# Optimization experiments

Hardware: AMD Instinct MI355X
Metric: run time of the kernel (lower is better)

Reference implementation:

```python
import jax, jax.numpy as jnp
import numpy as np

H = 256          # hidden_dim
B = 64           # molecules
M = 64           # atoms per molecule (equal-size molecules)
N = B * M        # total nodes
NE = 119         # element classes
NB = 5           # bond classes
EPS = 1e-5
OFF_I, OFF_J = np.where(~np.eye(M, dtype=bool))  # static off-diagonal pair order (i-major, j!=i)


def _gelu(x):
    return jax.nn.gelu(x, approximate=False)


def _ln(x, g, b):
    mu = jnp.mean(x, axis=-1, keepdims=True)
    var = jnp.mean((x - mu) ** 2, axis=-1, keepdims=True)
    return (x - mu) * jax.lax.rsqrt(var + EPS) * g + b


def _mlp(x, W1, b1, g, bn, W2, b2, W3, b3):
    x = _gelu(x @ W1 + b1)
    x = _ln(x, g, bn)
    x = _gelu(x @ W2 + b2)
    return x @ W3 + b3


def setup_inputs():
    key = jax.random.key(0)
    ks = jax.random.split(key, 16)
    s = 0.02
    def lin(k, fi, fo):
        return jax.random.normal(k, (fi, fo), jnp.float32) * s
    inp = {}
    inp["h"] = jax.random.normal(ks[0], (N, H), jnp.float32)
    inp["pos"] = jax.random.normal(ks[1], (N, 3), jnp.float32) * 3.0
    inp["edge_index"] = jax.random.randint(ks[2], (2, N * 8), 0, N)
    inp["batch"] = jnp.repeat(jnp.arange(B), M)
    # atom_predictor params
    inp["aW1"] = lin(ks[3], H, H); inp["ab1"] = jnp.zeros((H,))
    inp["ag"] = jnp.ones((H,)); inp["abn"] = jnp.zeros((H,))
    inp["aW2"] = lin(ks[4], H, H // 2); inp["ab2"] = jnp.zeros((H // 2,))
    inp["aW3"] = lin(ks[5], H // 2, NE); inp["ab3"] = jnp.zeros((NE,))
    # valency_predictor params
    inp["vW1"] = lin(ks[6], H + NE, H); inp["vb1"] = jnp.zeros((H,))
    inp["vg"] = jnp.ones((H,)); inp["vbn"] = jnp.zeros((H,))
    inp["vW2"] = lin(ks[7], H, H // 2); inp["vb2"] = jnp.zeros((H // 2,))
    inp["vW3"] = lin(ks[8], H // 2, 1); inp["vb3"] = jnp.zeros((1,))
    # bond_predictor params
    inp["bW1"] = lin(ks[9], 2 * H + 4, H); inp["bb1"] = jnp.zeros((H,))
    inp["bg"] = jnp.ones((H,)); inp["bbn"] = jnp.zeros((H,))
    inp["bW2"] = lin(ks[10], H, H // 2); inp["bb2"] = jnp.zeros((H // 2,))
    inp["bW3"] = lin(ks[11], H // 2, NB); inp["bb3"] = jnp.zeros((NB,))
    # chemical constant buffers (stand-ins for RDKit tables)
    mv = np.ones(NE, np.float32) * 4.0
    mv[[1, 9, 17, 35, 53]] = 1.0; mv[8] = 2.0; mv[7] = 3.0; mv[16] = 6.0; mv[15] = 5.0
    inp["max_valences"] = jnp.asarray(mv)
    cr = np.ones(NE, np.float32) * 1.5
    cr[1] = 0.31; cr[6] = 0.76; cr[7] = 0.71; cr[8] = 0.66; cr[9] = 0.57; cr[16] = 1.05
    inp["covalent_radii"] = jnp.asarray(cr)
    return inp


def _forward(h, pos, aW1, ab1, ag, abn, aW2, ab2, aW3, ab3,
             vW1, vb1, vg, vbn, vW2, vb2, vW3, vb3,
             bW1, bb1, bg, bbn, bW2, bb2, bW3, bb3,
             max_valences, covalent_radii):
    atom_logits = _mlp(h, aW1, ab1, ag, abn, aW2, ab2, aW3, ab3)        # [N,119]
    atom_probs = jax.nn.softmax(atom_logits, axis=-1)
    val = _mlp(jnp.concatenate([h, atom_probs], -1), vW1, vb1, vg, vbn, vW2, vb2, vW3, vb3)
    val = jax.nn.softplus(val)                                          # [N,1]
    pred = jnp.clip(jnp.argmax(atom_probs, -1), 0, 118)
    max_allowed = max_valences[pred]                                    # [N]
    # torch.min([N], [N,1]) broadcasts to [N,N] in the original -- reproduced faithfully
    valency_constrained = jnp.minimum(val[:, 0], max_allowed[:, None])  # [N,N]
    # vectorized pairwise bond prediction per molecule (equal-size molecules)
    hB = h.reshape(B, M, H)
    pB = pos.reshape(B, M, 3)
    probsB = atom_probs.reshape(B, M, NE)
    dist = jnp.linalg.norm(pB[:, :, None, :] - pB[:, None, :, :], axis=-1)  # [B,M,M]
    radii = covalent_radii[jnp.minimum(jnp.argmax(probsB, -1), 118)]        # [B,M]
    expected = radii[:, :, None] + radii[:, None, :]                        # [B,M,M]
    close = (dist < 3.0).astype(h.dtype)
    feats = jnp.concatenate([
        jnp.broadcast_to(hB[:, :, None, :], (B, M, M, H)),
        jnp.broadcast_to(hB[:, None, :, :], (B, M, M, H)),
        dist[..., None], expected[..., None],
        (dist / expected)[..., None], close[..., None],
    ], axis=-1)                                                             # [B,M,M,2H+4]
    logits = _mlp(feats, bW1, bb1, bg, bbn, bW2, bb2, bW3, bb3)             # [B,M,M,5]
    probs5 = jax.nn.softmax(logits, axis=-1)
    e0 = jnp.zeros((NB,), h.dtype).at[0].set(1.0)
    diag = jnp.eye(M, dtype=bool)[None, :, :, None]
    adjacency = jnp.where(diag, e0, probs5)                                 # [B,M,M,5]
    bond_logits = logits[:, OFF_I, OFF_J, :].reshape(B * M * (M - 1), NB)   # skip i==j, i-major order
    return (atom_logits, bond_logits, valency_constrained, adjacency)


def reference(h, pos, edge_index, batch, aW1, ab1, ag, abn, aW2, ab2, aW3, ab3,
              vW1, vb1, vg, vbn, vW2, vb2, vW3, vb3,
              bW1, bb1, bg, bbn, bW2, bb2, bW3, bb3, max_valences, covalent_radii):
    # edge_index is unused by the original forward; batch is implicit in the [B,M] layout
    return _forward(h, pos, aW1, ab1, ag, abn, aW2, ab2, aW3, ab3,
                    vW1, vb1, vg, vbn, vW2, vb2, vW3, vb3,
                    bW1, bb1, bg, bbn, bW2, bb2, bW3, bb3,
                    max_valences, covalent_radii)
```

## Files before the change

### kernel.cpp

```cpp
#include <hip/hip_runtime.h>
#include <math.h>

#define NN   4096
#define HH   256
#define NEC  119
#define NBC  5

#define OFF_ATOM   0
#define OFF_BOND   487424
#define OFF_VALM   (487424+1290240)
#define OFF_ADJ    (1777664+16777216)

typedef short  bf16x8 __attribute__((ext_vector_type(8)));
typedef float  f32x4  __attribute__((ext_vector_type(4)));

__device__ __forceinline__ float gelu_f(float x) {
    float z = fabsf(x) * 0.70710678118654752f;
    float t = __builtin_amdgcn_rcpf(fmaf(0.3275911f, z, 1.0f));
    float p = t * fmaf(t, fmaf(t, fmaf(t, fmaf(t, 1.061405429f, -1.453152027f),
                                       1.421413741f), -0.284496736f), 0.254829592f);
    float er = fmaf(-p, __expf(-z * z), 1.0f);
    float s = copysignf(er, x);
    return 0.5f * x * (1.f + s);
}
__device__ __forceinline__ unsigned short f2bf(float x) {
    unsigned int u = __float_as_uint(x);
    unsigned int r = (u + 0x7fffu + ((u >> 16) & 1u)) >> 16;
    return (unsigned short)r;
}

__global__ __launch_bounds__(256) void k_prep(
    const float* __restrict__ bW1, const float* __restrict__ bW2,
    const float* __restrict__ bW3, const float* __restrict__ vW1,
    const float* __restrict__ vW2,
    const float* __restrict__ bg, const float* __restrict__ bbn,
    const float* __restrict__ bb2,
    short* __restrict__ PQf, short* __restrict__ V1f, short* __restrict__ V2vf,
    short* __restrict__ W2f, short* __restrict__ W3f,
    float* __restrict__ uu, float* __restrict__ vvb)
{
    const int t = threadIdx.x;
    if (blockIdx.x == 1160) {
        if (t < 128) {
            float ua = 0.f, va = 0.f;
            for (int c = 0; c < 256; ++c) {
                float w = bW2[c * 128 + t];
                ua = fmaf(bg[c],  w, ua);
                va = fmaf(bbn[c], w, va);
            }
            uu[t]  = ua;
            vvb[t] = va + bb2[t];
        }
        return;
    }
    const int id = blockIdx.x * 256 + t;
    if (id < 131072) {
        const int e = id & 7, l = (id >> 3) & 63;
        const int rem = id >> 9, ks = rem & 7, ct = rem >> 3;
        const int k = ks * 32 + (l >> 4) * 8 + e;
        const int col = ct * 16 + (l & 15);
        float v = (col < 256) ? bW1[k * 256 + col] : bW1[(256 + k) * 256 + (col - 256)];
        PQf[id] = (short)f2bf(v);
    } else if (id < 229376) {
        const int id2 = id - 131072;
        const int e = id2 & 7, l = (id2 >> 3) & 63;
        const int rem = id2 >> 9, ks = rem % 12, ct = rem / 12;
        const int kk = ks * 32 + (l >> 4) * 8 + e;
        const int col = ct * 16 + (l & 15);
        V1f[id2] = (kk < 375) ? (short)f2bf(vW1[kk * 256 + col]) : (short)0;
    } else if (id < 262144) {
        const int id3 = id - 229376;
        const int e = id3 & 7, l = (id3 >> 3) & 63;
        const int rem = id3 >> 9, ks = rem & 7, ct = rem >> 3;
        const int k = ks * 32 + (l >> 4) * 8 + e;
        const int col = ct * 16 + (l & 15);
        V2vf[id3] = (short)f2bf(vW2[k * 128 + col]);
    } else if (id < 294912) {
        const int id4 = id - 262144;
        const int e = id4 & 7, l = (id4 >> 3) & 63;
        const int ks = (id4 >> 9) & 7, ct = (id4 >> 12) & 7;
        const int k = ks * 32 + (l >> 4) * 8 + e;
        const int col = ct * 16 + (l & 15);
        W2f[id4] = (short)f2bf(bW2[k * 128 + col]);
    } else if (id < 296960) {
        const int id5 = id - 294912;
        const int e = id5 & 7, l = (id5 >> 3) & 63, ks = id5 >> 9;
        const int k = ks * 32 + (l >> 4) * 8 + e;
        const int col = l & 15;
        W3f[id5] = (col < NBC) ? (short)f2bf(bW3[k * NBC + col]) : (short)0;
    }
}

__global__ __launch_bounds__(256, 3) void k_front(
    const float* __restrict__ h,
    const float* __restrict__ aW1, const float* __restrict__ ab1,
    const float* __restrict__ ag,  const float* __restrict__ abn,
    const float* __restrict__ aW2, const float* __restrict__ ab2,
    const float* __restrict__ aW3, const float* __restrict__ ab3,
    const float* __restrict__ maxv, const float* __restrict__ covr,
    const float* __restrict__ vb1, const float* __restrict__ vg,
    const float* __restrict__ vbn, const float* __restrict__ vb2,
    const float* __restrict__ vW3, const float* __restrict__ vb3,
    const float* __restrict__ bb1,
    const short* __restrict__ PQf, const short* __restrict__ V1f,
    const short* __restrict__ V2vf,
    float* __restrict__ logits_out,
    float* __restrict__ ma, float* __restrict__ rad, float* __restrict__ val,
    float* __restrict__ P, float* __restrict__ Q)
{
    __shared__ __align__(16) char smem[44864];
    float (*hs)[256]   = (float(*)[256])(smem);
    unsigned short* hb = (unsigned short*)(smem + 8192);
    float (*z1)[256]   = (float(*)[256])(smem + 20480);
    float (*z2)[128]   = (float(*)[128])(smem + 28672);
    float (*llog)[120] = (float(*)[120])(smem + 32768);
    unsigned short* zb = (unsigned short*)(smem + 36608);
    float (*redbuf)[2] = (float(*)[2])(smem + 44800);

    const int t  = threadIdx.x;
    const int wv = t >> 6, ln = t & 63;
    const int lr = ln & 15, kg = ln >> 4;

    if (blockIdx.x >= 512) {
        unsigned short* hbq = (unsigned short*)smem;
        const int gb  = blockIdx.x - 512;
        const int rt  = gb & 63, ct4 = gb >> 6;
        const int n0  = rt * 64, c0 = ct4 * 64;

        for (int i = 0; i < 16; ++i) {
            const int idx4 = t + 256 * i;
            const int r = idx4 >> 6, k4 = (idx4 & 63) * 4;
            float4 hv = *(const float4*)(h + (size_t)(n0 + r) * 256 + k4);
            ushort4 u;
            u.x = f2bf(hv.x); u.y = f2bf(hv.y); u.z = f2bf(hv.z); u.w = f2bf(hv.w);
            const int off = r * 512 + ((((k4 >> 3) ^ (r & 7))) << 4) + ((k4 & 7) << 1);
            *(ushort4*)((char*)hbq + off) = u;
        }
        __syncthreads();

        const int wr0 = wv * 16;
        f32x4 acc[4];
        #pragma unroll
        for (int ctl = 0; ctl < 4; ++ctl) acc[ctl] = (f32x4){0.f, 0.f, 0.f, 0.f};
        #pragma unroll
        for (int ks = 0; ks < 8; ++ks) {
            const int row = wr0 + lr;
            const int chunk = ks * 4 + kg;
            const int aoff = row * 512 + ((chunk ^ (row & 7)) << 4);
            bf16x8 afr = *(const bf16x8*)((char*)hbq + aoff);
            #pragma unroll
            for (int ctl = 0; ctl < 4; ++ctl) {
                const int ct_pq = ct4 * 4 + ctl;
                bf16x8 bfr = *(const bf16x8*)(PQf + (((size_t)(ct_pq * 8 + ks)) * 64 + ln) * 8);
                acc[ctl] = __builtin_amdgcn_mfma_f32_16x16x32_bf16(afr, bfr, acc[ctl], 0, 0, 0);
            }
        }
        #pragma unroll
        for (int ctl = 0; ctl < 4; ++ctl) {
            const int colg = c0 + ctl * 16 + lr;
            const float bias = (colg < 256) ? bb1[colg] : 0.f;
            #pragma unroll
            for (int r = 0; r < 4; ++r) {
                const int n = n0 + wr0 + kg * 4 + r;
                float v = acc[ctl][r] + bias;
                if (colg < 256) P[(size_t)n * 256 + colg] = v;
                else            Q[(size_t)n * 256 + (colg - 256)] = v;
            }
        }
        return;
    }

    const int n0 = blockIdx.x * 8;

    #pragma unroll
    for (int i = 0; i < 3; ++i)
        *(int4*)((char*)hb + (t + 256 * i) * 16) = (int4){0, 0, 0, 0};
    *(int4*)((char*)zb + 4096 + t * 16) = (int4){0, 0, 0, 0};
    for (int i = 0; i < 2; ++i) {
        const int idx4 = t + 256 * i;
        const int r = idx4 >> 6, k4 = (idx4 & 63) * 4;
        float4 hv = *(const float4*)(h + (size_t)(n0 + r) * 256 + k4);
        *(float4*)&hs[r][k4] = hv;
        ushort4 u;
        u.x = f2bf(hv.x); u.y = f2bf(hv.y); u.z = f2bf(hv.z); u.w = f2bf(hv.w);
        const int off = r * 768 + ((((k4 >> 3) ^ (r & 7))) << 4) + ((k4 & 7) << 1);
        *(ushort4*)((char*)hb + off) = u;
    }
    __syncthreads();

    {
        const int c = t;
        float b1 = ab1[c];
        float acc[8];
        #pragma unroll
        for (int r = 0; r < 8; ++r) acc[r] = b1;
        for (int k4 = 0; k4 < 64; ++k4) {
            const int k = k4 * 4;
            float w0 = aW1[(k + 0) * 256 + c];
            float w1 = aW1[(k + 1) * 256 + c];
            float w2 = aW1[(k + 2) * 256 + c];
            float w3 = aW1[(k + 3) * 256 + c];
            #pragma unroll
            for (int r = 0; r < 8; ++r) {
                float4 hv = *(const float4*)&hs[r][k];
                acc[r] = fmaf(hv.x, w0, acc[r]);
                acc[r] = fmaf(hv.y, w1, acc[r]);
                acc[r] = fmaf(hv.z, w2, acc[r]);
                acc[r] = fmaf(hv.w, w3, acc[r]);
            }
        }
        #pragma unroll
        for (int r = 0; r < 8; ++r) z1[r][c] = gelu_f(acc[r]);
    }
    __syncthreads();

    for (int rr = 0; rr < 2; ++rr) {
        const int r = wv * 2 + rr;
        float s = 0.f, s2 = 0.f;
        #pragma unroll
        for (int q = 0; q < 4; ++q) {
            float v = z1[r][ln + q * 64];
            s += v; s2 = fmaf(v, v, s2);
        }
        #pragma unroll
        for (int m = 32; m >= 1; m >>= 1) {
            s  += __shfl_xor(s,  m, 64);
            s2 += __shfl_xor(s2, m, 64);
        }
        if (ln == 0) {
            float mu  = s * (1.f / 256.f);
            float var = s2 * (1.f / 256.f) - mu * mu;
            redbuf[r][0] = mu;
            redbuf[r][1] = rsqrtf(var + 1e-5f);
        }
    }
    __syncthreads();
    {
        const int c = t;
        float g = ag[c], b = abn[c];
        #pragma unroll
        for (int r = 0; r < 8; ++r)
            z1[r][c] = (z1[r][c] - redbuf[r][0]) * redbuf[r][1] * g + b;
    }
    __syncthreads();

    {
        const int c2 = t & 127, kh = t >> 7;
        float acc2[8];
        #pragma unroll
        for (int r = 0; r < 8; ++r) acc2[r] = 0.f;
        const int kb = kh * 128;
        for (int k4 = 0; k4 < 32; ++k4) {
            const int k = kb + k4 * 4;
            float w0 = aW2[(k + 0) * 128 + c2];
            float w1 = aW2[(k + 1) * 128 + c2];
            float w2 = aW2[(k + 2) * 128 + c2];
            float w3 = aW2[(k + 3) * 128 + c2];
            #pragma unroll
            for (int r = 0; r < 8; ++r) {
                float4 zv = *(const float4*)&z1[r][k];
                acc2[r] = fmaf(zv.x, w0, acc2[r]);
                acc2[r] = fmaf(zv.y, w1, acc2[r]);
                acc2[r] = fmaf(zv.z, w2, acc2[r]);
                acc2[r] = fmaf(zv.w, w3, acc2[r]);
            }
        }
        if (kh == 1) {
            #pragma unroll
            for (int r = 0; r < 8; ++r) z2[r][c2] = acc2[r];
        }
        __syncthreads();
        if (kh == 0) {
            float b2 = ab2[c2];
            #pragma unroll
            for (int r = 0; r < 8; ++r)
                z2[r][c2] = gelu_f(acc2[r] + z2[r][c2] + b2);
        }
    }
    __syncthreads();

    if (t < NEC) {
        const int c = t;
        float b3 = ab3[c];
        float acc3[8];
        #pragma unroll
        for (int r = 0; r < 8; ++r) acc3[r] = b3;
        for (int k4 = 0; k4 < 32; ++k4) {
            const int k = k4 * 4;
            float w0 = aW3[(k + 0) * NEC + c];
            float w1 = aW3[(k + 1) * NEC + c];
            float w2 = aW3[(k + 2) * NEC + c];
            float w3 = aW3[(k + 3) * NEC + c];
            #pragma unroll
            for (int r = 0; r < 8; ++r) {
                float4 zv = *(const float4*)&z2[r][k];
                acc3[r] = fmaf(zv.x, w0, acc3[r]);
                acc3[r] = fmaf(zv.y, w1, acc3[r]);
                acc3[r] = fmaf(zv.z, w2, acc3[r]);
                acc3[r] = fmaf(zv.w, w3, acc3[r]);
            }
        }
        #pragma unroll
        for (int r = 0; r < 8; ++r) {
            llog[r][c] = acc3[r];
            logits_out[(size_t)(n0 + r) * NEC + c] = acc3[r];
        }
    }
    __syncthreads();

    for (int rr = 0; rr < 2; ++rr) {
        const int r = wv * 2 + rr;
        float v1 = llog[r][ln];
        float v2 = (ln + 64 < NEC) ? llog[r][ln + 64] : -1e30f;
        float mx; int mi;
        if (v2 > v1) { mx = v2; mi = ln + 64; } else { mx = v1; mi = ln; }
        #pragma unroll
        for (int m = 32; m >= 1; m >>= 1) {
            float ov = __shfl_xor(mx, m, 64);
            int   oi = __shfl_xor(mi, m, 64);
            if (ov > mx || (ov == mx && oi < mi)) { mx = ov; mi = oi; }
        }
        float e1 = __expf(v1 - mx);
        float e2 = (ln + 64 < NEC) ? __expf(v2 - mx) : 0.f;
        float s = e1 + e2;
        #pragma unroll
        for (int m = 32; m >= 1; m >>= 1) s += __shfl_xor(s, m, 64);
        float inv = __builtin_amdgcn_rcpf(s);
        {
            const int cf = 256 + ln;
            const int off = r * 768 + ((((cf >> 3) ^ (r & 7))) << 4) + ((cf & 7) << 1);
            *(unsigned short*)((char*)hb + off) = f2bf(e1 * inv);
        }
        if (ln + 64 < NEC) {
            const int cf = 256 + ln + 64;
            const int off = r * 768 + ((((cf >> 3) ^ (r & 7))) << 4) + ((cf & 7) << 1);
            *(unsigned short*)((char*)hb + off) = f2bf(e2 * inv);
        }
        if (ln == 0) {
            ma[n0 + r]  = maxv[mi];
            rad[n0 + r] = covr[mi];
        }
    }
    __syncthreads();

    {
        f32x4 acc[4];
        #pragma unroll
        for (int ctl = 0; ctl < 4; ++ctl) acc[ctl] = (f32x4){0.f, 0.f, 0.f, 0.f};
        #pragma unroll
        for (int ks = 0; ks < 12; ++ks) {
            const int row = lr;
            const int chunk = ks * 4 + kg;
            const int aoff = row * 768 + ((chunk ^ (row & 7)) << 4);
            bf16x8 afr = *(const bf16x8*)((char*)hb + aoff);
            #pragma unroll
            for (int ctl = 0; ctl < 4; ++ctl) {
                const int ctg = wv * 4 + ctl;
                bf16x8 bfr = *(const bf16x8*)(V1f + (((size_t)(ctg * 12 + ks)) * 64 + ln) * 8);
                acc[ctl] = __builtin_amdgcn_mfma_f32_16x16x32_bf16(afr, bfr, acc[ctl], 0, 0, 0);
            }
        }
        if (kg < 2) {
            #pragma unroll
            for (int ctl = 0; ctl < 4; ++ctl) {
                const int col = (wv * 4 + ctl) * 16 + lr;
                const float b1 = vb1[col];
                #pragma unroll
                for (int r = 0; r < 4; ++r)
                    z1[kg * 4 + r][col] = gelu_f(acc[ctl][r] + b1);
            }
        }
    }
    __syncthreads();

    for (int rr = 0; rr < 2; ++rr) {
        const int r = wv * 2 + rr;
        float s = 0.f, s2 = 0.f;
        #pragma unroll
        for (int q = 0; q < 4; ++q) {
            float v = z1[r][ln + q * 64];
            s += v; s2 = fmaf(v, v, s2);
        }
        #pragma unroll
        for (int m = 32; m >= 1; m >>= 1) {
            s  += __shfl_xor(s,  m, 64);
            s2 += __shfl_xor(s2, m, 64);
        }
        if (ln == 0) {
            float mu  = s * (1.f / 256.f);
            float var = s2 * (1.f / 256.f) - mu * mu;
            redbuf[r][0] = mu;
            redbuf[r][1] = rsqrtf(var + 1e-5f);
        }
    }
    __syncthreads();
    {
        const int c = t;
        float g = vg[c], b = vbn[c];
        #pragma unroll
        for (int r = 0; r < 8; ++r) {
            float v = (z1[r][c] - redbuf[r][0]) * redbuf[r][1] * g + b;
            const int off = r * 512 + ((((c >> 3) ^ (r & 7))) << 4) + ((c & 7) << 1);
            *(unsigned short*)((char*)zb + off) = f2bf(v);
        }
    }
    __syncthreads();

    {
        f32x4 acc2[2];
        #pragma unroll
        for (int c2 = 0; c2 < 2; ++c2) acc2[c2] = (f32x4){0.f, 0.f, 0.f, 0.f};
        #pragma unroll
        for (int ks = 0; ks < 8; ++ks) {
            const int row = lr;
            const int chunk = ks * 4 + kg;
            const int aoff = row * 512 + ((chunk ^ (row & 7)) << 4);
            bf16x8 afr = *(const bf16x8*)((char*)zb + aoff);
            #pragma unroll
            for (int c2 = 0; c2 < 2; ++c2) {
                const int ctg = wv * 2 + c2;
                bf16x8 bfr = *(const bf16x8*)(V2vf + (((size_t)(ctg * 8 + ks)) * 64 + ln) * 8);
                acc2[c2] = __builtin_amdgcn_mfma_f32_16x16x32_bf16(afr, bfr, acc2[c2], 0, 0, 0);
            }
        }
        if (kg < 2) {
            #pragma unroll
            for (int c2 = 0; c2 < 2; ++c2) {
                const int col = (wv * 2 + c2) * 16 + lr;
                const float b2 = vb2[col];
                #pragma unroll
                for (int r = 0; r < 4; ++r)
                    z2[kg * 4 + r][col] = gelu_f(acc2[c2][r] + b2);
            }
        }
    }
    __syncthreads();

    for (int rr = 0; rr < 2; ++rr) {
        const int r = wv * 2 + rr;
        float p = fmaf(z2[r][ln], vW3[ln], z2[r][ln + 64] * vW3[ln + 64]);
        #pragma unroll
        for (int m = 32; m >= 1; m >>= 1) p += __shfl_xor(p, m, 64);
        if (ln == 0) {
            float x = p + vb3[0];
            val[n0 + r] = (x > 15.f) ? x : log1pf(expf(x));
        }
    }
}

__global__ __launch_bounds__(256, 4) void k_back(
    const float* __restrict__ pos, const float* __restrict__ rad,
    const float* __restrict__ P, const float* __restrict__ Q,
    const float* __restrict__ bW1, const float* __restrict__ bg,
    const short* __restrict__ W2f, const short* __restrict__ W3f,
    const float* __restrict__ bb3,
    const float* __restrict__ uu, const float* __restrict__ vvb,
    const float* __restrict__ val, const float* __restrict__ ma,
    float* __restrict__ bond_logits, float* __restrict__ adjacency,
    float* __restrict__ valmat)
{
    __shared__ float posr[64][4];
    __shared__ float Pis[256];
    __shared__ float wst0[256], wst1[256], wst2[256], wst3[256];
    __shared__ float gams[256];
    __shared__ float us_[128], vbs[128];
    __shared__ unsigned short Ys[64 * 128];
    __shared__ float Ls[64][5];

    const int t  = threadIdx.x;

    if (blockIdx.x >= 4096) {
        const int i0 = (blockIdx.x - 4096) * 8;
        const float4* v4 = (const float4*)val;
        for (int rr = 0; rr < 8; ++rr) {
            const int i = i0 + rr;
            const float mi = ma[i];
            float4* o4 = (float4*)(valmat + (size_t)i * 4096);
            for (int j = t; j < 1024; j += 256) {
                float4 v = v4[j];
                float4 r;
                r.x = fminf(v.x, mi); r.y = fminf(v.y, mi);
                r.z = fminf(v.z, mi); r.w = fminf(v.w, mi);
                o4[j] = r;
            }
        }
        return;
    }

    const int bi = blockIdx.x;
    const int b  = bi >> 6, i = bi & 63;
    const int wv = t >> 6, ln = t & 63;
    const int lr = ln & 15, kg = ln >> 4;
    const int node0 = b * 64;
    const int j = wv * 16 + lr;

    if (t < 64) {
        int n = node0 + t;
        posr[t][0] = pos[n * 3 + 0];
        posr[t][1] = pos[n * 3 + 1];
        posr[t][2] = pos[n * 3 + 2];
        posr[t][3] = rad[n];
    }
    Pis[t]  = P[(size_t)(node0 + i) * 256 + t];
    wst0[t] = bW1[(size_t)512 * 256 + t];
    wst1[t] = bW1[(size_t)513 * 256 + t];
    wst2[t] = bW1[(size_t)514 * 256 + t];
    wst3[t] = bW1[(size_t)515 * 256 + t];
    gams[t] = bg[t];
    if (t < 128) { us_[t] = uu[t]; vbs[t] = vvb[t]; }
    __syncthreads();

    float dx = posr[i][0] - posr[j][0];
    float dy = posr[i][1] - posr[j][1];
    float dz = posr[i][2] - posr[j][2];
    float dist  = sqrtf(fmaf(dx, dx, fmaf(dy, dy, dz * dz)));
    float expd  = posr[i][3] + posr[j][3];
    float ratio = dist * __builtin_amdgcn_rcpf(expd);
    float close = (dist < 3.f) ? 1.f : 0.f;

    float s = 0.f, s2 = 0.f;
    bf16x8 afr[8];
    const float* Qrow = Q + (size_t)(node0 + j) * 256;
    #pragma unroll
    for (int ks = 0; ks < 8; ++ks) {
        const int base = ks * 32 + kg * 8;
        float4 Pa  = *(const float4*)&Pis[base],  Pb  = *(const float4*)&Pis[base + 4];
        float4 Qa  = *(const float4*)(Qrow + base), Qb = *(const float4*)(Qrow + base + 4);
        float4 w0a = *(const float4*)&wst0[base], w0b = *(const float4*)&wst0[base + 4];
        float4 w1a = *(const float4*)&wst1[base], w1b = *(const float4*)&wst1[base + 4];
        float4 w2a = *(const float4*)&wst2[base], w2b = *(const float4*)&wst2[base + 4];
        float4 w3a = *(const float4*)&wst3[base], w3b = *(const float4*)&wst3[base + 4];
        float4 ga  = *(const float4*)&gams[base], gb  = *(const float4*)&gams[base + 4];
        float g, xg;
        #define LANECH(P_, Q_, W0_, W1_, W2_, W3_, G_, EI) \
            g = P_ + Q_; g = fmaf(W0_, dist, g); g = fmaf(W1_, expd, g); \
            g = fmaf(W2_, ratio, g); g = fmaf(W3_, close, g); g = gelu_f(g); \
            s += g; s2 = fmaf(g, g, s2); xg = g * G_; afr[ks][EI] = (short)f2bf(xg);
        LANECH(Pa.x, Qa.x, w0a.x, w1a.x, w2a.x, w3a.x, ga.x, 0)
        LANECH(Pa.y, Qa.y, w0a.y, w1a.y, w2a.y, w3a.y, ga.y, 1)
        LANECH(Pa.z, Qa.z, w0a.z, w1a.z, w2a.z, w3a.z, ga.z, 2)
        LANECH(Pa.w, Qa.w, w0a.w, w1a.w, w2a.w, w3a.w, ga.w, 3)
        LANECH(Pb.x, Qb.x, w0b.x, w1b.x, w2b.x, w3b.x, gb.x, 4)
        LANECH(Pb.y, Qb.y, w0b.y, w1b.y, w2b.y, w3b.y, gb.y, 5)
        LANECH(Pb.z, Qb.z, w0b.z, w1b.z, w2b.z, w3b.z, gb.z, 6)
        LANECH(Pb.w, Qb.w, w0b.w, w1b.w, w2b.w, w3b.w, gb.w, 7)
        #undef LANECH
    }
    s  += __shfl_xor(s,  16, 64);  s  += __shfl_xor(s,  32, 64);
    s2 += __shfl_xor(s2, 16, 64);  s2 += __shfl_xor(s2, 32, 64);
    const float mu   = s * (1.f / 256.f);
    const float rstd = rsqrtf(s2 * (1.f / 256.f) - mu * mu + 1e-5f);

    f32x4 acc[8];
    #pragma unroll
    for (int ct = 0; ct < 8; ++ct) acc[ct] = (f32x4){0.f, 0.f, 0.f, 0.f};
    #pragma unroll
    for (int ks = 0; ks < 8; ++ks) {
        #pragma unroll
        for (int ct = 0; ct < 8; ++ct) {
            bf16x8 bfr = *(const bf16x8*)(W2f + (((size_t)(ct * 8 + ks)) * 64 + ln) * 8);
            acc[ct] = __builtin_amdgcn_mfma_f32_16x16x32_bf16(afr[ks], bfr, acc[ct], 0, 0, 0);
        }
    }

    float rst[4], rm[4];
    #pragma unroll
    for (int r = 0; r < 4; ++r) {
        float sr = __shfl(rstd, kg * 4 + r, 64);
        float mr = __shfl(mu,   kg * 4 + r, 64);
        rst[r] = sr; rm[r] = sr * mr;
    }
    #pragma unroll
    for (int ct = 0; ct < 8; ++ct) {
        const int col = ct * 16 + lr;
        const float ucv = us_[col], vcv = vbs[col];
        #pragma unroll
        for (int r = 0; r < 4; ++r) {
            float y = fmaf(rst[r], acc[ct][r], fmaf(-rm[r], ucv, vcv));
            y = gelu_f(y);
            const int row = wv * 16 + kg * 4 + r;
            const int chunk = col >> 3;
            const int off = row * 256 + ((chunk ^ (row & 7)) << 4) + ((col & 7) << 1);
            *(unsigned short*)((char*)Ys + off) = f2bf(y);
        }
    }

    {
        f32x4 acc3 = (f32x4){0.f, 0.f, 0.f, 0.f};
        #pragma unroll
        for (int ks = 0; ks < 4; ++ks) {
            bf16x8 bfr = *(const bf16x8*)(W3f + ((size_t)(ks * 64 + ln)) * 8);
            const int row   = wv * 16 + lr;
            const int chunk = ks * 4 + kg;
            const int off   = row * 256 + ((chunk ^ (row & 7)) << 4);
            bf16x8 afr2 = *(const bf16x8*)((char*)Ys + off);
            acc3 = __builtin_amdgcn_mfma_f32_16x16x32_bf16(afr2, bfr, acc3, 0, 0, 0);
        }
        if (lr < NBC) {
            #pragma unroll
            for (int r = 0; r < 4; ++r)
                Ls[wv * 16 + kg * 4 + r][lr] = acc3[r];
        }
    }

    const size_t adjbase  = (size_t)bi * 64 * 5;
    const size_t bondbase = ((size_t)b * 4032 + (size_t)i * 63) * 5;
    const float b30 = bb3[0], b31 = bb3[1], b32 = bb3[2], b33 = bb3[3], b34 = bb3[4];
    for (int u = ln; u < 80; u += 64) {
        const int jl = u / 5, o = u - jl * 5;
        const int j2 = wv * 16 + jl;
        float l0 = Ls[j2][0] + b30, l1 = Ls[j2][1] + b31, l2 = Ls[j2][2] + b32;
        float l3 = Ls[j2][3] + b33, l4 = Ls[j2][4] + b34;
        float mx = fmaxf(fmaxf(fmaxf(l0, l1), fmaxf(l2, l3)), l4);
        float e0 = __expf(l0 - mx), e1 = __expf(l1 - mx), e2 = __expf(l2 - mx);
        float e3 = __expf(l3 - mx), e4 = __expf(l4 - mx);
        float inv = __builtin_amdgcn_rcpf(e0 + e1 + e2 + e3 + e4);
        float lo = (o == 0) ? l0 : (o == 1) ? l1 : (o == 2) ? l2 : (o == 3) ? l3 : l4;
        float po = ((o == 0) ? e0 : (o == 1) ? e1 : (o == 2) ? e2 : (o == 3) ? e3 : e4) * inv;
        adjacency[adjbase + (size_t)j2 * 5 + o] = (j2 == i) ? ((o == 0) ? 1.f : 0.f) : po;
        if (j2 != i) {
            const int jj = j2 - (j2 > i ? 1 : 0);
            bond_logits[bondbase + (size_t)jj * 5 + o] = lo;
        }
    }
}

extern "C" void kernel_launch(void* const* d_in, const int* in_sizes, int n_in,
                              void* d_out, int out_size, void* d_ws, size_t ws_size,
                              hipStream_t stream)
{
    (void)in_sizes; (void)n_in; (void)out_size; (void)ws_size;
    const float* h   = (const float*)d_in[0];
    const float* pos = (const float*)d_in[1];
    const float* aW1 = (const float*)d_in[4];
    const float* ab1 = (const float*)d_in[5];
    const float* ag  = (const float*)d_in[6];
    const float* abn = (const float*)d_in[7];
    const float* aW2 = (const float*)d_in[8];
    const float* ab2 = (const float*)d_in[9];
    const float* aW3 = (const float*)d_in[10];
    const float* ab3 = (const float*)d_in[11];
    const float* vW1 = (const float*)d_in[12];
    const float* vb1 = (const float*)d_in[13];
    const float* vg  = (const float*)d_in[14];
    const float* vbn = (const float*)d_in[15];
    const float* vW2 = (const float*)d_in[16];
    const float* vb2 = (const float*)d_in[17];
    const float* vW3 = (const float*)d_in[18];
    const float* vb3 = (const float*)d_in[19];
    const float* bW1 = (const float*)d_in[20];
    const float* bb1 = (const float*)d_in[21];
    const float* bg  = (const float*)d_in[22];
    const float* bbn = (const float*)d_in[23];
    const float* bW2 = (const float*)d_in[24];
    const float* bb2 = (const float*)d_in[25];
    const float* bW3 = (const float*)d_in[26];
    const float* bb3 = (const float*)d_in[27];
    const float* mv  = (const float*)d_in[28];
    const float* cr  = (const float*)d_in[29];

    float* out = (float*)d_out;
    float* atom_logits = out + OFF_ATOM;
    float* bond_logits = out + OFF_BOND;
    float* valmat      = out + OFF_VALM;
    float* adjacency   = out + OFF_ADJ;

    float* ws    = (float*)d_ws;
    float* ma    = ws;
    float* rad   = ws + 4096;
    float* val   = ws + 8192;
    float* Pp    = ws + 12288;
    float* Qq    = ws + 1060864;
    float* uu    = ws + 2109440;
    float* vvb   = ws + 2109568;
    short* W2f   = (short*)(ws + 2109696);
    short* W3f   = (short*)(ws + 2126080);
    short* PQf   = (short*)(ws + 2127104);
    short* V1f   = (short*)(ws + 2192640);
    short* V2vf  = (short*)(ws + 2241792);

    k_prep<<<1161, 256, 0, stream>>>(bW1, bW2, bW3, vW1, vW2, bg, bbn, bb2,
                                     PQf, V1f, V2vf, W2f, W3f, uu, vvb);
    k_front<<<1024, 256, 0, stream>>>(h,
        aW1, ab1, ag, abn, aW2, ab2, aW3, ab3, mv, cr,
        vb1, vg, vbn, vb2, vW3, vb3, bb1,
        PQf, V1f, V2vf,
        atom_logits, ma, rad, val, Pp, Qq);
    k_back<<<4608, 256, 0, stream>>>(pos, rad, Pp, Qq, bW1, bg,
                                     W2f, W3f, bb3, uu, vvb, val, ma,
                                     bond_logits, adjacency, valmat);
}
```

Baseline: 299.4 us.

## Move atom predictor MLP to split-bf16 MFMA with 16-row tiles

The atom predictor's three scalar fp32 GEMMs are replaced with bf16 MFMA using a hi/lo split (hi*hi + hi*lo + lo*hi) to keep near-fp32 accuracy. Weights are pre-split and pre-swizzled in the prep kernel. Front blocks now process 16 rows instead of 8, halving those blocks, with shared memory regrown accordingly. Occupancy hints change: front drops to 2 blocks per CU and back rises to 6. The split approach costs three MFMAs per tile and extra prep work, and the larger shared memory footprint lowers front occupancy.

```diff
diff --git a/kernel.cpp b/kernel.cpp
--- a/kernel.cpp
+++ b/kernel.cpp
@@ -28,19 +28,27 @@
     unsigned int r = (u + 0x7fffu + ((u >> 16) & 1u)) >> 16;
     return (unsigned short)r;
 }
+__device__ __forceinline__ float bf2f(unsigned short s) {
+    return __uint_as_float(((unsigned int)s) << 16);
+}
 
 __global__ __launch_bounds__(256) void k_prep(
     const float* __restrict__ bW1, const float* __restrict__ bW2,
     const float* __restrict__ bW3, const float* __restrict__ vW1,
     const float* __restrict__ vW2,
+    const float* __restrict__ aW1, const float* __restrict__ aW2,
+    const float* __restrict__ aW3,
     const float* __restrict__ bg, const float* __restrict__ bbn,
     const float* __restrict__ bb2,
     short* __restrict__ PQf, short* __restrict__ V1f, short* __restrict__ V2vf,
     short* __restrict__ W2f, short* __restrict__ W3f,
+    short* __restrict__ A1h, short* __restrict__ A1l,
+    short* __restrict__ A2h, short* __restrict__ A2l,
+    short* __restrict__ A3h, short* __restrict__ A3l,
     float* __restrict__ uu, float* __restrict__ vvb)
 {
     const int t = threadIdx.x;
-    if (blockIdx.x == 1160) {
+    if (blockIdx.x == 2056) {
         if (t < 128) {
             float ua = 0.f, va = 0.f;
             for (int c = 0; c < 256; ++c) {
@@ -88,15 +96,50 @@
         const int k = ks * 32 + (l >> 4) * 8 + e;
         const int col = l & 15;
         W3f[id5] = (col < NBC) ? (short)f2bf(bW3[k * NBC + col]) : (short)0;
+    } else if (id < 428032) {
+        const int id6 = id - 296960;
+        const int half = (id6 >= 65536);
+        const int id7 = id6 & 65535;
+        const int e = id7 & 7, l = (id7 >> 3) & 63;
+        const int rem = id7 >> 9, ks = rem & 7, ct = rem >> 3;
+        const int k = ks * 32 + (l >> 4) * 8 + e;
+        const int col = ct * 16 + (l & 15);
+        float w = aW1[k * 256 + col];
+        unsigned short hi = f2bf(w);
+        if (!half) A1h[id7] = (short)hi;
+        else       A1l[id7] = (short)f2bf(w - bf2f(hi));
+    } else if (id < 493568) {
+        const int id6 = id - 428032;
+        const int half = (id6 >= 32768);
+        const int id7 = id6 & 32767;
+        const int e = id7 & 7, l = (id7 >> 3) & 63;
+        const int rem = id7 >> 9, ks = rem & 7, ct = rem >> 3;
+        const int k = ks * 32 + (l >> 4) * 8 + e;
+        const int col = ct * 16 + (l & 15);
+        float w = aW2[k * 128 + col];
+        unsigned short hi = f2bf(w);
+        if (!half) A2h[id7] = (short)hi;
+        else       A2l[id7] = (short)f2bf(w - bf2f(hi));
+    } else if (id < 526336) {
+        const int id6 = id - 493568;
+        const int half = (id6 >= 16384);
+        const int id7 = id6 & 16383;
+        const int e = id7 & 7, l = (id7 >> 3) & 63;
+        const int rem = id7 >> 9, ks = rem & 3, ct = rem >> 2;
+        const int k = ks * 32 + (l >> 4) * 8 + e;
+        const int col = ct * 16 + (l & 15);
+        float w = (col < NEC) ? aW3[k * NEC + col] : 0.f;
+        unsigned short hi = f2bf(w);
+        if (!half) A3h[id7] = (short)hi;
+        else       A3l[id7] = (short)f2bf(w - bf2f(hi));
     }
 }
 
-__global__ __launch_bounds__(256, 3) void k_front(
+__global__ __launch_bounds__(256, 2) void k_front(
     const float* __restrict__ h,
-    const float* __restrict__ aW1, const float* __restrict__ ab1,
-    const float* __restrict__ ag,  const float* __restrict__ abn,
-    const float* __restrict__ aW2, const float* __restrict__ ab2,
-    const float* __restrict__ aW3, const float* __restrict__ ab3,
+    const float* __restrict__ ab1, const float* __restrict__ ag,
+    const float* __restrict__ abn, const float* __restrict__ ab2,
+    const float* __restrict__ ab3,
     const float* __restrict__ maxv, const float* __restrict__ covr,
     const float* __restrict__ vb1, const float* __restrict__ vg,
     const float* __restrict__ vbn, const float* __restrict__ vb2,
@@ -104,26 +147,33 @@
     const float* __restrict__ bb1,
     const short* __restrict__ PQf, const short* __restrict__ V1f,
     const short* __restrict__ V2vf,
+    const short* __restrict__ A1h, const short* __restrict__ A1l,
+    const short* __restrict__ A2h, const short* __restrict__ A2l,
+    const short* __restrict__ A3h, const short* __restrict__ A3l,
     float* __restrict__ logits_out,
     float* __restrict__ ma, float* __restrict__ rad, float* __restrict__ val,
     float* __restrict__ P, float* __restrict__ Q)
 {
-    __shared__ __align__(16) char smem[44864];
-    float (*hs)[256]   = (float(*)[256])(smem);
-    unsigned short* hb = (unsigned short*)(smem + 8192);
-    float (*z1)[256]   = (float(*)[256])(smem + 20480);
-    float (*z2)[128]   = (float(*)[128])(smem + 28672);
-    float (*llog)[120] = (float(*)[120])(smem + 32768);
-    unsigned short* zb = (unsigned short*)(smem + 36608);
-    float (*redbuf)[2] = (float(*)[2])(smem + 44800);
+    __shared__ __align__(16) char smem[61568];
+    unsigned short* hb   = (unsigned short*)(smem);
+    unsigned short* hlob = (unsigned short*)(smem + 12288);
+    float*          z1f  = (float*)(smem + 20480);
+    unsigned short* z1lo = (unsigned short*)(smem + 36864);
+    float*          z2f  = (float*)(smem + 45056);
+    unsigned short* z2hi = (unsigned short*)(smem + 53248);
+    unsigned short* z2lo = (unsigned short*)(smem + 57344);
+    float (*redbuf)[2]   = (float(*)[2])(smem + 61440);
+    float*          llog = (float*)(smem + 20480);
+    unsigned short* z1hi = hlob;
+    unsigned short* zb   = z1lo;
 
     const int t  = threadIdx.x;
     const int wv = t >> 6, ln = t & 63;
     const int lr = ln & 15, kg = ln >> 4;
 
-    if (blockIdx.x >= 512) {
+    if (blockIdx.x >= 256) {
         unsigned short* hbq = (unsigned short*)smem;
-        const int gb  = blockIdx.x - 512;
+        const int gb  = blockIdx.x - 256;
         const int rt  = gb & 63, ct4 = gb >> 6;
         const int n0  = rt * 64, c0 = ct4 * 64;
 
@@ -170,56 +220,66 @@
         return;
     }
 
-    const int n0 = blockIdx.x * 8;
-
-    #pragma unroll
-    for (int i = 0; i < 3; ++i)
-        *(int4*)((char*)hb + (t + 256 * i) * 16) = (int4){0, 0, 0, 0};
-    *(int4*)((char*)zb + 4096 + t * 16) = (int4){0, 0, 0, 0};
-    for (int i = 0; i < 2; ++i) {
+    const int n0 = blockIdx.x * 16;
+
+    for (int i = 0; i < 4; ++i) {
         const int idx4 = t + 256 * i;
         const int r = idx4 >> 6, k4 = (idx4 & 63) * 4;
         float4 hv = *(const float4*)(h + (size_t)(n0 + r) * 256 + k4);
-        *(float4*)&hs[r][k4] = hv;
-        ushort4 u;
-        u.x = f2bf(hv.x); u.y = f2bf(hv.y); u.z = f2bf(hv.z); u.w = f2bf(hv.w);
-        const int off = r * 768 + ((((k4 >> 3) ^ (r & 7))) << 4) + ((k4 & 7) << 1);
-        *(ushort4*)((char*)hb + off) = u;
+        ushort4 uh, ul;
+        uh.x = f2bf(hv.x); ul.x = f2bf(hv.x - bf2f(uh.x));
+        uh.y = f2bf(hv.y); ul.y = f2bf(hv.y - bf2f(uh.y));
+        uh.z = f2bf(hv.z); ul.z = f2bf(hv.z - bf2f(uh.z));
+        uh.w = f2bf(hv.w); ul.w = f2bf(hv.w - bf2f(uh.w));
+        const int sw = ((k4 >> 3) ^ (r & 7)) << 4;
+        const int sub = (k4 & 7) << 1;
+        *(ushort4*)((char*)hb   + r * 768 + sw + sub) = uh;
+        *(ushort4*)((char*)hlob + r * 512 + sw + sub) = ul;
+    }
+    for (int idx = t; idx < 144; idx += 256) {
+        const int r = idx / 9, c = 375 + (idx % 9);
+        const int off = r * 768 + ((((c >> 3) ^ (r & 7))) << 4) + ((c & 7) << 1);
+        *(unsigned short*)((char*)hb + off) = 0;
     }
     __syncthreads();
 
     {
-        const int c = t;
-        float b1 = ab1[c];
-        float acc[8];
-        #pragma unroll
-        for (int r = 0; r < 8; ++r) acc[r] = b1;
-        for (int k4 = 0; k4 < 64; ++k4) {
-            const int k = k4 * 4;
-            float w0 = aW1[(k + 0) * 256 + c];
-            float w1 = aW1[(k + 1) * 256 + c];
-            float w2 = aW1[(k + 2) * 256 + c];
-            float w3 = aW1[(k + 3) * 256 + c];
-            #pragma unroll
-            for (int r = 0; r < 8; ++r) {
-                float4 hv = *(const float4*)&hs[r][k];
-                acc[r] = fmaf(hv.x, w0, acc[r]);
-                acc[r] = fmaf(hv.y, w1, acc[r]);
-                acc[r] = fmaf(hv.z, w2, acc[r]);
-                acc[r] = fmaf(hv.w, w3, acc[r]);
-            }
-        }
-        #pragma unroll
-        for (int r = 0; r < 8; ++r) z1[r][c] = gelu_f(acc[r]);
-    }
-    __syncthreads();
-
-    for (int rr = 0; rr < 2; ++rr) {
-        const int r = wv * 2 + rr;
+        f32x4 acc[4];
+        #pragma unroll
+        for (int ctl = 0; ctl < 4; ++ctl) acc[ctl] = (f32x4){0.f, 0.f, 0.f, 0.f};
+        #pragma unroll
+        for (int ks = 0; ks < 8; ++ks) {
+            const int chunk = ks * 4 + kg;
+            const int sw = (chunk ^ (lr & 7)) << 4;
+            bf16x8 ahi = *(const bf16x8*)((char*)hb   + lr * 768 + sw);
+            bf16x8 alo = *(const bf16x8*)((char*)hlob + lr * 512 + sw);
+            #pragma unroll
+            for (int ctl = 0; ctl < 4; ++ctl) {
+                const int ctg = wv * 4 + ctl;
+                bf16x8 bhi = *(const bf16x8*)(A1h + (((size_t)(ctg * 8 + ks)) * 64 + ln) * 8);
+                bf16x8 blo = *(const bf16x8*)(A1l + (((size_t)(ctg * 8 + ks)) * 64 + ln) * 8);
+                acc[ctl] = __builtin_amdgcn_mfma_f32_16x16x32_bf16(ahi, bhi, acc[ctl], 0, 0, 0);
+                acc[ctl] = __builtin_amdgcn_mfma_f32_16x16x32_bf16(ahi, blo, acc[ctl], 0, 0, 0);
+                acc[ctl] = __builtin_amdgcn_mfma_f32_16x16x32_bf16(alo, bhi, acc[ctl], 0, 0, 0);
+            }
+        }
+        #pragma unroll
+        for (int ctl = 0; ctl < 4; ++ctl) {
+            const int col = (wv * 4 + ctl) * 16 + lr;
+            const float b1 = ab1[col];
+            #pragma unroll
+            for (int r = 0; r < 4; ++r)
+                z1f[(kg * 4 + r) * 256 + col] = gelu_f(acc[ctl][r] + b1);
+        }
+    }
+    __syncthreads();
+
+    for (int rr = 0; rr < 4; ++rr) {
+        const int r = wv * 4 + rr;
         float s = 0.f, s2 = 0.f;
         #pragma unroll
         for (int q = 0; q < 4; ++q) {
-            float v = z1[r][ln + q * 64];
+            float v = z1f[r * 256 + ln + q * 64];
             s += v; s2 = fmaf(v, v, s2);
         }
         #pragma unroll
@@ -238,80 +298,97 @@
     {
         const int c = t;
         float g = ag[c], b = abn[c];
-        #pragma unroll
-        for (int r = 0; r < 8; ++r)
-            z1[r][c] = (z1[r][c] - redbuf[r][0]) * redbuf[r][1] * g + b;
+        for (int r = 0; r < 16; ++r) {
+            float v = (z1f[r * 256 + c] - redbuf[r][0]) * redbuf[r][1] * g + b;
+            unsigned short hi = f2bf(v);
+            unsigned short lo = f2bf(v - bf2f(hi));
+            const int off = r * 512 + ((((c >> 3) ^ (r & 7))) << 4) + ((c & 7) << 1);
+            *(unsigned short*)((char*)z1hi + off) = hi;
+            *(unsigned short*)((char*)z1lo + off) = lo;
+        }
     }
     __syncthreads();
 
     {
-        const int c2 = t & 127, kh = t >> 7;
-        float acc2[8];
-        #pragma unroll
-        for (int r = 0; r < 8; ++r) acc2[r] = 0.f;
-        const int kb = kh * 128;
-        for (int k4 = 0; k4 < 32; ++k4) {
-            const int k = kb + k4 * 4;
-            float w0 = aW2[(k + 0) * 128 + c2];
-            float w1 = aW2[(k + 1) * 128 + c2];
-            float w2 = aW2[(k + 2) * 128 + c2];
-            float w3 = aW2[(k + 3) * 128 + c2];
-            #pragma unroll
-            for (int r = 0; r < 8; ++r) {
-                float4 zv = *(const float4*)&z1[r][k];
-                acc2[r] = fmaf(zv.x, w0, acc2[r]);
-                acc2[r] = fmaf(zv.y, w1, acc2[r]);
-                acc2[r] = fmaf(zv.z, w2, acc2[r]);
-                acc2[r] = fmaf(zv.w, w3, acc2[r]);
-            }
-        }
-        if (kh == 1) {
-            #pragma unroll
-            for (int r = 0; r < 8; ++r) z2[r][c2] = acc2[r];
+        f32x4 acc2[2];
+        #pragma unroll
+        for (int c2 = 0; c2 < 2; ++c2) acc2[c2] = (f32x4){0.f, 0.f, 0.f, 0.f};
+        #pragma unroll
+        for (int ks = 0; ks < 8; ++ks) {
+            const int chunk = ks * 4 + kg;
+            const int sw = (chunk ^ (lr & 7)) << 4;
+            bf16x8 ahi = *(const bf16x8*)((char*)z1hi + lr * 512 + sw);
+            bf16x8 alo = *(const bf16x8*)((char*)z1lo + lr * 512 + sw);
+            #pragma unroll
+            for (int c2 = 0; c2 < 2; ++c2) {
+                const int ctg = wv * 2 + c2;
+                bf16x8 bhi = *(const bf16x8*)(A2h + (((size_t)(ctg * 8 + ks)) * 64 + ln) * 8);
+                bf16x8 blo = *(const bf16x8*)(A2l + (((size_t)(ctg * 8 + ks)) * 64 + ln) * 8);
+                acc2[c2] = __builtin_amdgcn_mfma_f32_16x16x32_bf16(ahi, bhi, acc2[c2], 0, 0, 0);
+                acc2[c2] = __builtin_amdgcn_mfma_f32_16x16x32_bf16(ahi, blo, acc2[c2], 0, 0, 0);
+                acc2[c2] = __builtin_amdgcn_mfma_f32_16x16x32_bf16(alo, bhi, acc2[c2], 0, 0, 0);
+            }
+        }
+        #pragma unroll
+        for (int c2 = 0; c2 < 2; ++c2) {
+            const int col = (wv * 2 + c2) * 16 + lr;
+            const float b2 = ab2[col];
+            #pragma unroll
+            for (int r = 0; r < 4; ++r) {
+                float y = gelu_f(acc2[c2][r] + b2);
+                unsigned short hi = f2bf(y);
+                unsigned short lo = f2bf(y - bf2f(hi));
+                const int row = kg * 4 + r;
+                const int off = row * 256 + ((((col >> 3) ^ (row & 7))) << 4) + ((col & 7) << 1);
+                *(unsigned short*)((char*)z2hi + off) = hi;
+                *(unsigned short*)((char*)z2lo + off) = lo;
+            }
+        }
+    }
+    __syncthreads();
+
+    {
+        f32x4 acc3[2];
+        #pragma unroll
+        for (int c2 = 0; c2 < 2; ++c2) acc3[c2] = (f32x4){0.f, 0.f, 0.f, 0.f};
+        #pragma unroll
+        for (int ks = 0; ks < 4; ++ks) {
+            const int chunk = ks * 4 + kg;
+            const int sw = (chunk ^ (lr & 7)) << 4;
+            bf16x8 ahi = *(const bf16x8*)((char*)z2hi + lr * 256 + sw);
+            bf16x8 alo = *(const bf16x8*)((char*)z2lo + lr * 256 + sw);
+            #pragma unroll
+            for (int c2 = 0; c2 < 2; ++c2) {
+                const int ctg = wv * 2 + c2;
+                bf16x8 bhi = *(const bf16x8*)(A3h + (((size_t)(ctg * 4 + ks)) * 64 + ln) * 8);
+                bf16x8 blo = *(const bf16x8*)(A3l + (((size_t)(ctg * 4 + ks)) * 64 + ln) * 8);
+                acc3[c2] = __builtin_amdgcn_mfma_f32_16x16x32_bf16(ahi, bhi, acc3[c2], 0, 0, 0);
+                acc3[c2] = __builtin_amdgcn_mfma_f32_16x16x32_bf16(ahi, blo, acc3[c2], 0, 0, 0);
+                acc3[c2] = __builtin_amdgcn_mfma_f32_16x16x32_bf16(alo, bhi, acc3[c2], 0, 0, 0);
+            }
         }
         __syncthreads();
-        if (kh == 0) {
-            float b2 = ab2[c2];
-            #pragma unroll
-            for (int r = 0; r < 8; ++r)
-                z2[r][c2] = gelu_f(acc2[r] + z2[r][c2] + b2);
-        }
-    }
-    __syncthreads();
-
-    if (t < NEC) {
-        const int c = t;
-        float b3 = ab3[c];
-        float acc3[8];
-        #pragma unroll
-        for (int r = 0; r < 8; ++r) acc3[r] = b3;
-        for (int k4 = 0; k4 < 32; ++k4) {
-            const int k = k4 * 4;
-            float w0 = aW3[(k + 0) * NEC + c];
-            float w1 = aW3[(k + 1) * NEC + c];
-            float w2 = aW3[(k + 2) * NEC + c];
-            float w3 = aW3[(k + 3) * NEC + c];
-            #pragma unroll
-            for (int r = 0; r < 8; ++r) {
-                float4 zv = *(const float4*)&z2[r][k];
-                acc3[r] = fmaf(zv.x, w0, acc3[r]);
-                acc3[r] = fmaf(zv.y, w1, acc3[r]);
-                acc3[r] = fmaf(zv.z, w2, acc3[r]);
-                acc3[r] = fmaf(zv.w, w3, acc3[r]);
-            }
-        }
-        #pragma unroll
-        for (int r = 0; r < 8; ++r) {
-            llog[r][c] = acc3[r];
-            logits_out[(size_t)(n0 + r) * NEC + c] = acc3[r];
-        }
-    }
-    __syncthreads();
-
-    for (int rr = 0; rr < 2; ++rr) {
-        const int r = wv * 2 + rr;
-        float v1 = llog[r][ln];
-        float v2 = (ln + 64 < NEC) ? llog[r][ln + 64] : -1e30f;
+        #pragma unroll
+        for (int c2 = 0; c2 < 2; ++c2) {
+            const int col = (wv * 2 + c2) * 16 + lr;
+            if (col < NEC) {
+                const float b3 = ab3[col];
+                #pragma unroll
+                for (int r = 0; r < 4; ++r) {
+                    const int row = kg * 4 + r;
+                    float v = acc3[c2][r] + b3;
+                    llog[row * 120 + col] = v;
+                    logits_out[(size_t)(n0 + row) * NEC + col] = v;
+                }
+            }
+        }
+    }
+    __syncthreads();
+
+    for (int rr = 0; rr < 4; ++rr) {
+        const int r = wv * 4 + rr;
+        float v1 = llog[r * 120 + ln];
+        float v2 = (ln + 64 < NEC) ? llog[r * 120 + ln + 64] : -1e30f;
         float mx; int mi;
         if (v2 > v1) { mx = v2; mi = ln + 64; } else { mx = v1; mi = ln; }
         #pragma unroll
@@ -349,10 +426,8 @@
         for (int ctl = 0; ctl < 4; ++ctl) acc[ctl] = (f32x4){0.f, 0.f, 0.f, 0.f};
         #pragma unroll
         for (int ks = 0; ks < 12; ++ks) {
-            const int row = lr;
             const int chunk = ks * 4 + kg;
-            const int aoff = row * 768 + ((chunk ^ (row & 7)) << 4);
-            bf16x8 afr = *(const bf16x8*)((char*)hb + aoff);
+            bf16x8 afr = *(const bf16x8*)((char*)hb + lr * 768 + ((chunk ^ (lr & 7)) << 4));
             #pragma unroll
             for (int ctl = 0; ctl < 4; ++ctl) {
                 const int ctg = wv * 4 + ctl;
@@ -360,25 +435,24 @@
                 acc[ctl] = __builtin_amdgcn_mfma_f32_16x16x32_bf16(afr, bfr, acc[ctl], 0, 0, 0);
             }
         }
-        if (kg < 2) {
-            #pragma unroll
-            for (int ctl = 0; ctl < 4; ++ctl) {
-                const int col = (wv * 4 + ctl) * 16 + lr;
-                const float b1 = vb1[col];
-                #pragma unroll
-                for (int r = 0; r < 4; ++r)
-                    z1[kg * 4 + r][col] = gelu_f(acc[ctl][r] + b1);
-            }
-        }
-    }
-    __syncthreads();
-
-    for (int rr = 0; rr < 2; ++rr) {
-        const int r = wv * 2 + rr;
+        __syncthreads();
+        #pragma unroll
+        for (int ctl = 0; ctl < 4; ++ctl) {
+            const int col = (wv * 4 + ctl) * 16 + lr;
+            const float b1 = vb1[col];
+            #pragma unroll
+            for (int r = 0; r < 4; ++r)
+                z1f[(kg * 4 + r) * 256 + col] = gelu_f(acc[ctl][r] + b1);
+        }
+    }
+    __syncthreads();
+
+    for (int rr = 0; rr < 4; ++rr) {
+        const int r = wv * 4 + rr;
         float s = 0.f, s2 = 0.f;
         #pragma unroll
         for (int q = 0; q < 4; ++q) {
-            float v = z1[r][ln + q * 64];
+            float v = z1f[r * 256 + ln + q * 64];
             s += v; s2 = fmaf(v, v, s2);
         }
         #pragma unroll
@@ -397,9 +471,8 @@
     {
         const int c = t;
         float g = vg[c], b = vbn[c];
-        #pragma unroll
-        for (int r = 0; r < 8; ++r) {
-            float v = (z1[r][c] - redbuf[r][0]) * redbuf[r][1] * g + b;
+        for (int r = 0; r < 16; ++r) {
+            float v = (z1f[r * 256 + c] - redbuf[r][0]) * redbuf[r][1] * g + b;
             const int off = r * 512 + ((((c >> 3) ^ (r & 7))) << 4) + ((c & 7) << 1);
             *(unsigned short*)((char*)zb + off) = f2bf(v);
         }
@@ -412,10 +485,8 @@
         for (int c2 = 0; c2 < 2; ++c2) acc2[c2] = (f32x4){0.f, 0.f, 0.f, 0.f};
         #pragma unroll
         for (int ks = 0; ks < 8; ++ks) {
-            const int row = lr;
             const int chunk = ks * 4 + kg;
-            const int aoff = row * 512 + ((chunk ^ (row & 7)) << 4);
-            bf16x8 afr = *(const bf16x8*)((char*)zb + aoff);
+            bf16x8 afr = *(const bf16x8*)((char*)zb + lr * 512 + ((chunk ^ (lr & 7)) << 4));
             #pragma unroll
             for (int c2 = 0; c2 < 2; ++c2) {
                 const int ctg = wv * 2 + c2;
@@ -423,22 +494,20 @@
                 acc2[c2] = __builtin_amdgcn_mfma_f32_16x16x32_bf16(afr, bfr, acc2[c2], 0, 0, 0);
             }
         }
-        if (kg < 2) {
-            #pragma unroll
-            for (int c2 = 0; c2 < 2; ++c2) {
-                const int col = (wv * 2 + c2) * 16 + lr;
-                const float b2 = vb2[col];
-                #pragma unroll
-                for (int r = 0; r < 4; ++r)
-                    z2[kg * 4 + r][col] = gelu_f(acc2[c2][r] + b2);
-            }
-        }
-    }
-    __syncthreads();
-
-    for (int rr = 0; rr < 2; ++rr) {
-        const int r = wv * 2 + rr;
-        float p = fmaf(z2[r][ln], vW3[ln], z2[r][ln + 64] * vW3[ln + 64]);
+        #pragma unroll
+        for (int c2 = 0; c2 < 2; ++c2) {
+            const int col = (wv * 2 + c2) * 16 + lr;
+            const float b2 = vb2[col];
+            #pragma unroll
+            for (int r = 0; r < 4; ++r)
+                z2f[(kg * 4 + r) * 128 + col] = gelu_f(acc2[c2][r] + b2);
+        }
+    }
+    __syncthreads();
+
+    for (int rr = 0; rr < 4; ++rr) {
+        const int r = wv * 4 + rr;
+        float p = fmaf(z2f[r * 128 + ln], vW3[ln], z2f[r * 128 + ln + 64] * vW3[ln + 64]);
         #pragma unroll
         for (int m = 32; m >= 1; m >>= 1) p += __shfl_xor(p, m, 64);
         if (ln == 0) {
@@ -448,7 +517,7 @@
     }
 }
 
-__global__ __launch_bounds__(256, 4) void k_back(
+__global__ __launch_bounds__(256, 6) void k_back(
     const float* __restrict__ pos, const float* __restrict__ rad,
     const float* __restrict__ P, const float* __restrict__ Q,
     const float* __restrict__ bW1, const float* __restrict__ bg,
@@ -678,13 +747,21 @@
     short* PQf   = (short*)(ws + 2127104);
     short* V1f   = (short*)(ws + 2192640);
     short* V2vf  = (short*)(ws + 2241792);
-
-    k_prep<<<1161, 256, 0, stream>>>(bW1, bW2, bW3, vW1, vW2, bg, bbn, bb2,
-                                     PQf, V1f, V2vf, W2f, W3f, uu, vvb);
-    k_front<<<1024, 256, 0, stream>>>(h,
-        aW1, ab1, ag, abn, aW2, ab2, aW3, ab3, mv, cr,
+    short* A1h   = (short*)(ws + 2258176);
+    short* A1l   = (short*)(ws + 2290944);
+    short* A2h   = (short*)(ws + 2323712);
+    short* A2l   = (short*)(ws + 2340096);
+    short* A3h   = (short*)(ws + 2356480);
+    short* A3l   = (short*)(ws + 2364672);
+
+    k_prep<<<2057, 256, 0, stream>>>(bW1, bW2, bW3, vW1, vW2, aW1, aW2, aW3,
+                                     bg, bbn, bb2,
+                                     PQf, V1f, V2vf, W2f, W3f,
+                                     A1h, A1l, A2h, A2l, A3h, A3l, uu, vvb);
+    k_front<<<768, 256, 0, stream>>>(h,
+        ab1, ag, abn, ab2, ab3, mv, cr,
         vb1, vg, vbn, vb2, vW3, vb3, bb1,
-        PQf, V1f, V2vf,
+        PQf, V1f, V2vf, A1h, A1l, A2h, A2l, A3h, A3l,
         atom_logits, ma, rad, val, Pp, Qq);
     k_back<<<4608, 256, 0, stream>>>(pos, rad, Pp, Qq, bW1, bg,
                                      W2f, W3f, bb3, uu, vvb, val, ma,
```

Result: slower. 306.1 us (+2.2%).
